# Kernel optimization log

Measured on AMD Instinct MI355X. Metric: run time of the kernel, lower is better.

## Reference

```python
import jax, jax.numpy as jnp
import numpy as np

U = 128        # operand extent (multiplicity of the single mode 'u')
NSEG = 4       # num_segments for each of the 3 operands
NPATH = 20     # number of CG paths
BATCH = 100000 # batch (e.g. number of edges)


def setup_inputs() -> dict:
    key = jax.random.key(0)
    k0, k1, k2, k3 = jax.random.split(key, 4)
    x0 = jax.random.normal(k0, (BATCH, NSEG * U), dtype=jnp.float32)
    x1 = jax.random.normal(k1, (BATCH, NSEG * U), dtype=jnp.float32)
    path_indices = jax.random.randint(k2, (NPATH, 3), 0, NSEG, dtype=jnp.int32)
    path_coefficients = jax.random.normal(k3, (NPATH,), dtype=jnp.float32)
    return {
        "x0": x0,
        "x1": x1,
        "path_coefficients": path_coefficients,
        "path_indices": path_indices,
    }


def reference(x0, x1, path_coefficients, path_indices):
    # Segmented uniform-1d tensor product (subscripts 'u,u,u', no coefficient
    # subscripts): for each path p with indices (i0, i1, i2) and scalar coef c_p,
    # out[:, i2, :] += c_p * x0[:, i0, :] * x1[:, i1, :]
    B = x0.shape[0]
    s0 = x0.reshape(B, NSEG, U)
    s1 = x1.reshape(B, NSEG, U)
    i0, i1, i2 = path_indices[:, 0], path_indices[:, 1], path_indices[:, 2]
    g0 = s0[:, i0, :]  # [B, P, U] gather of input-0 segments per path
    g1 = s1[:, i1, :]  # [B, P, U]
    prod = path_coefficients[None, :, None] * g0 * g1  # [B, P, U]
    # scatter-add paths into output segments
    out = jax.ops.segment_sum(prod.transpose(1, 0, 2), i2, num_segments=NSEG)  # [NSEG, B, U]
    return out.transpose(1, 0, 2).reshape(B, NSEG * U)
```

## Files before the change

### kernel.cpp

```cpp
#include <hip/hip_runtime.h>

#define U 128
#define UV 32
#define NSEG 4
#define NPATH 20
#define ROW (NSEG * UV)

__global__ void build_w_kernel(const float* __restrict__ coef,
                               const int* __restrict__ idx,
                               float* __restrict__ W) {
    int j = threadIdx.x;
    if (j >= 64) return;
    int s2 = j >> 4;
    int a  = (j >> 2) & 3;
    int b  = j & 3;
    float w = 0.0f;
    for (int p = 0; p < NPATH; ++p) {
        int i0 = idx[p * 3 + 0];
        int i1 = idx[p * 3 + 1];
        int i2 = idx[p * 3 + 2];
        if (i0 == a && i1 == b && i2 == s2) w += coef[p];
    }
    W[j] = w;
}

__global__ __launch_bounds__(256) void tp_main_kernel(const float4* __restrict__ x0,
                                                      const float4* __restrict__ x1,
                                                      const float* __restrict__ W,
                                                      float4* __restrict__ out,
                                                      int total) {
    int t = blockIdx.x * 256 + threadIdx.x;
    if (t >= total) return;
    int b = t >> 5;
    int u = t & 31;
    int base = b * ROW + u;

    float4 a[NSEG], c[NSEG];
#pragma unroll
    for (int s = 0; s < NSEG; ++s) a[s] = x0[base + s * UV];
#pragma unroll
    for (int s = 0; s < NSEG; ++s) c[s] = x1[base + s * UV];

#pragma unroll
    for (int s2 = 0; s2 < NSEG; ++s2) {
        float4 acc = make_float4(0.f, 0.f, 0.f, 0.f);
#pragma unroll
        for (int aa = 0; aa < NSEG; ++aa) {
            float4 tv = make_float4(0.f, 0.f, 0.f, 0.f);
#pragma unroll
            for (int bb = 0; bb < NSEG; ++bb) {
                float wv = W[s2 * 16 + aa * 4 + bb];
                tv.x = fmaf(wv, c[bb].x, tv.x);
                tv.y = fmaf(wv, c[bb].y, tv.y);
                tv.z = fmaf(wv, c[bb].z, tv.z);
                tv.w = fmaf(wv, c[bb].w, tv.w);
            }
            acc.x = fmaf(a[aa].x, tv.x, acc.x);
            acc.y = fmaf(a[aa].y, tv.y, acc.y);
            acc.z = fmaf(a[aa].z, tv.z, acc.z);
            acc.w = fmaf(a[aa].w, tv.w, acc.w);
        }
        out[base + s2 * UV] = acc;
    }
}

extern "C" void kernel_launch(void* const* d_in, const int* in_sizes, int n_in,
                              void* d_out, int out_size, void* d_ws, size_t ws_size,
                              hipStream_t stream) {
    const float* x0   = (const float*)d_in[0];
    const float* x1   = (const float*)d_in[1];
    const float* coef = (const float*)d_in[2];
    const int*   idx  = (const int*)d_in[3];
    float* W = (float*)d_ws;

    int batch = in_sizes[0] / (NSEG * U);
    int total = batch * UV;

    build_w_kernel<<<1, 64, 0, stream>>>(coef, idx, W);
    tp_main_kernel<<<(total + 255) / 256, 256, 0, stream>>>(
        (const float4*)x0, (const float4*)x1, W, (float4*)d_out, total);
}
```

Before: 459.4 us.

## Use persistent grid-stride loop with register double-buffered prefetch of inputs

The main kernel now runs on a fixed grid of at most 2048 blocks. Each thread loops over several work items and issues the global loads for the next item before computing and storing the current one. This is meant to hide memory latency and cut block launch overhead. The cost is extra registers for the prefetch buffers, which may lower occupancy.

Result: no change. 462.7 us (+0.7%).

```diff
diff --git a/kernel.cpp b/kernel.cpp
--- a/kernel.cpp
+++ b/kernel.cpp
@@ -24,23 +24,21 @@
     W[j] = w;
 }
 
-__global__ __launch_bounds__(256) void tp_main_kernel(const float4* __restrict__ x0,
-                                                      const float4* __restrict__ x1,
-                                                      const float* __restrict__ W,
-                                                      float4* __restrict__ out,
-                                                      int total) {
-    int t = blockIdx.x * 256 + threadIdx.x;
-    if (t >= total) return;
-    int b = t >> 5;
-    int u = t & 31;
-    int base = b * ROW + u;
-
-    float4 a[NSEG], c[NSEG];
+__device__ __forceinline__ void tp_loads(const float4* __restrict__ x0,
+                                         const float4* __restrict__ x1,
+                                         int base,
+                                         float4 (&a)[NSEG], float4 (&c)[NSEG]) {
 #pragma unroll
     for (int s = 0; s < NSEG; ++s) a[s] = x0[base + s * UV];
 #pragma unroll
     for (int s = 0; s < NSEG; ++s) c[s] = x1[base + s * UV];
+}
 
+__device__ __forceinline__ void tp_compute_store(const float4 (&a)[NSEG],
+                                                 const float4 (&c)[NSEG],
+                                                 const float* __restrict__ W,
+                                                 float4* __restrict__ out,
+                                                 int base) {
 #pragma unroll
     for (int s2 = 0; s2 < NSEG; ++s2) {
         float4 acc = make_float4(0.f, 0.f, 0.f, 0.f);
@@ -64,6 +62,34 @@
     }
 }
 
+__global__ __launch_bounds__(256) void tp_main_kernel(const float4* __restrict__ x0,
+                                                      const float4* __restrict__ x1,
+                                                      const float* __restrict__ W,
+                                                      float4* __restrict__ out,
+                                                      int total) {
+    const int T = gridDim.x * 256;
+    int t = blockIdx.x * 256 + threadIdx.x;
+    if (t >= total) return;
+
+    float4 a[NSEG], c[NSEG], an[NSEG], cn[NSEG];
+    int base = (t >> 5) * ROW + (t & 31);
+    tp_loads(x0, x1, base, a, c);
+
+    for (;;) {
+        int tn = t + T;
+        bool more = tn < total;
+        int basen = (tn >> 5) * ROW + (tn & 31);
+        if (more) tp_loads(x0, x1, basen, an, cn);
+
+        tp_compute_store(a, c, W, out, base);
+
+        if (!more) break;
+        t = tn; base = basen;
+#pragma unroll
+        for (int s = 0; s < NSEG; ++s) { a[s] = an[s]; c[s] = cn[s]; }
+    }
+}
+
 extern "C" void kernel_launch(void* const* d_in, const int* in_sizes, int n_in,
                               void* d_out, int out_size, void* d_ws, size_t ws_size,
                               hipStream_t stream) {
@@ -76,7 +102,11 @@
     int batch = in_sizes[0] / (NSEG * U);
     int total = batch * UV;
 
+    int grid = 2048;
+    int need = (total + 255) / 256;
+    if (need < grid) grid = need;
+
     build_w_kernel<<<1, 64, 0, stream>>>(coef, idx, W);
-    tp_main_kernel<<<(total + 255) / 256, 256, 0, stream>>>(
+    tp_main_kernel<<<grid, 256, 0, stream>>>(
         (const float4*)x0, (const float4*)x1, W, (float4*)d_out, total);
 }
```
